# Kernel tuning notes

Measured on AMD Instinct MI355X. Metric: run time of the kernel, lower is better.

The kernel has to match this reference:

```python
import jax, jax.numpy as jnp
import numpy as np

N_NODES = 50000
N_EDGES = 800000
IN_CH = 128
OUT_CH = 128
TIME_DIM = 64


def setup_inputs() -> dict:
    key = jax.random.key(0)
    ks = jax.random.split(key, 7)
    x = jax.random.normal(ks[0], (N_NODES, IN_CH), dtype=jnp.float32)
    edge_index = jax.random.randint(ks[1], (2, N_EDGES), 0, N_NODES, dtype=jnp.int64)
    edge_t = jax.random.uniform(ks[2], (N_EDGES,), dtype=jnp.float32)
    # parameters
    freqs = jax.random.normal(ks[3], (TIME_DIM // 2,), dtype=jnp.float32)
    fan = IN_CH + TIME_DIM
    lim = float(np.sqrt(1.0 / fan))
    lin_w = jax.random.uniform(ks[4], (OUT_CH, fan), minval=-lim, maxval=lim, dtype=jnp.float32)
    lin_b = jax.random.uniform(ks[5], (OUT_CH,), minval=-lim, maxval=lim, dtype=jnp.float32)
    glim = float(np.sqrt(6.0 / (1 + OUT_CH)))
    attn = jax.random.uniform(ks[6], (1, OUT_CH), minval=-glim, maxval=glim, dtype=jnp.float32)
    return {"x": x, "edge_index": edge_index, "edge_t": edge_t,
            "freqs": freqs, "lin_w": lin_w, "lin_b": lin_b, "attn": attn}


def reference(x, edge_index, edge_t, freqs, lin_w, lin_b, attn):
    src, dst = edge_index[0], edge_index[1]
    n_nodes = x.shape[0]
    # time encoding: [E, time_dim]
    ang = edge_t[:, None] * freqs * (2.0 * jnp.pi)
    edge_attr = jnp.concatenate([jnp.sin(ang), jnp.cos(ang)], axis=-1)
    # gather source features and project: h = tanh(Linear(cat(x_j, te)))
    msg = jnp.concatenate([x[src], edge_attr], axis=-1)        # [E, in+time]
    h = jnp.tanh(msg @ lin_w.T + lin_b)                        # [E, out]
    # segment softmax over destination nodes
    alpha = (h * attn).sum(axis=-1)                            # [E]
    seg_max = jax.ops.segment_max(alpha, dst, num_segments=n_nodes)
    ex = jnp.exp(alpha - seg_max[dst])
    denom = jax.ops.segment_sum(ex, dst, num_segments=n_nodes)
    w = ex / (denom[dst] + 1e-16)
    # scatter-add aggregation
    out = jax.ops.segment_sum(h * w[:, None], dst, num_segments=n_nodes)
    return out
```

## Files before the change

kernel.cpp:

```cpp
#include <hip/hip_runtime.h>
#include <hip/hip_bf16.h>
#include <math.h>

#define IN_CHN 128
#define OUT_CHN 128
#define KD 192
#define TM 64

typedef __bf16 bf16x8 __attribute__((ext_vector_type(8)));
typedef float f32x4 __attribute__((ext_vector_type(4)));

static __device__ __forceinline__ unsigned short f2b(float f) {
    return __builtin_bit_cast(unsigned short, (__bf16)f);
}
static __device__ __forceinline__ float b2f(unsigned short b) {
    return __uint_as_float(((unsigned int)b) << 16);
}
static __device__ __forceinline__ float fast_tanh(float x) {
    float e = __expf(2.0f * x);
    return 1.0f - 2.0f * __builtin_amdgcn_rcpf(e + 1.0f);
}

#define GLL16(gsrc, ldst) \
    __builtin_amdgcn_global_load_lds( \
        (const __attribute__((address_space(1))) unsigned int*)(gsrc), \
        (__attribute__((address_space(3))) unsigned int*)(ldst), 16, 0, 0)

#define LDS_BARRIER() do { \
    asm volatile("s_waitcnt lgkmcnt(0)" ::: "memory"); \
    __builtin_amdgcn_s_barrier(); \
    __builtin_amdgcn_sched_barrier(0); \
} while (0)


__global__ __launch_bounds__(256) void cvt_x(const float* __restrict__ x,
    unsigned short* __restrict__ xb, long long n8)
{
    long long i = (long long)blockIdx.x * 256 + threadIdx.x;
    if (i >= n8) return;
    const float4* src = (const float4*)(x + i * 8);
    float4 v0 = src[0], v1 = src[1];
    ushort4 p0 = { f2b(v0.x), f2b(v0.y), f2b(v0.z), f2b(v0.w) };
    ushort4 p1 = { f2b(v1.x), f2b(v1.y), f2b(v1.z), f2b(v1.w) };
    *(ushort4*)(xb + i * 8)     = p0;
    *(ushort4*)(xb + i * 8 + 4) = p1;
}


__global__ __launch_bounds__(256) void count_deg(const int* __restrict__ ei,
                                                 int* __restrict__ deg, int E) {
    int e = blockIdx.x * 256 + threadIdx.x;
    if (e < E) atomicAdd(&deg[ei[E + e]], 1);
}

static __device__ __forceinline__ int wave_incl_scan(int v, int lane) {
    #pragma unroll
    for (int off = 1; off < 64; off <<= 1) {
        int t = __shfl_up(v, off);
        if (lane >= off) v += t;
    }
    return v;
}

__global__ __launch_bounds__(256) void scan_local(const int* __restrict__ deg,
    int* __restrict__ offs, int* __restrict__ partial, int Nn)
{
    __shared__ int wsum[4];
    int tid = threadIdx.x, lane = tid & 63, wid = tid >> 6;
    int i = blockIdx.x * 256 + tid;
    int v = (i < Nn) ? deg[i] : 0;
    int incl = wave_incl_scan(v, lane);
    if (lane == 63) wsum[wid] = incl;
    __syncthreads();
    int wpre = 0;
    for (int w = 0; w < wid; ++w) wpre += wsum[w];
    if (i < Nn) offs[i] = wpre + incl - v;
    if (tid == 255) partial[blockIdx.x] = wpre + incl;
}

__global__ __launch_bounds__(256) void scan_partial(int* __restrict__ partial, int nparts)
{
    __shared__ int wsum[4];
    int tid = threadIdx.x, lane = tid & 63, wid = tid >> 6;
    int v = (tid < nparts) ? partial[tid] : 0;
    int incl = wave_incl_scan(v, lane);
    if (lane == 63) wsum[wid] = incl;
    __syncthreads();
    int wpre = 0;
    for (int w = 0; w < wid; ++w) wpre += wsum[w];
    if (tid < nparts) partial[tid] = wpre + incl - v;
}

__global__ __launch_bounds__(256) void finalize_offs(int* __restrict__ offs,
    const int* __restrict__ partial, int* __restrict__ cursor, int Nn)
{
    int i = blockIdx.x * 256 + threadIdx.x;
    if (i < Nn) { int o = offs[i] + partial[i >> 8]; offs[i] = o; cursor[i] = o; }
}

__global__ __launch_bounds__(256) void fill_perm(const int* __restrict__ ei,
    const float* __restrict__ et, int* __restrict__ cursor,
    uint2* __restrict__ mt, int E)
{
    int e = blockIdx.x * 256 + threadIdx.x;
    if (e < E) {
        int d = ei[E + e];
        int pos = atomicAdd(&cursor[d], 1);
        mt[pos] = make_uint2((unsigned)ei[e], __float_as_uint(et[e]));
    }
}


__device__ __forceinline__ void load_meta(const uint2* __restrict__ mt,
    int tile, int E, int rbase, int g, int trow, int sv[2], float& tsv)
{
    int e0 = tile * TM;
    #pragma unroll
    for (int i = 0; i < 2; ++i) {
        int e = e0 + rbase + i * 4 + g;
        sv[i] = (int)mt[e < E ? e : E - 1].x;
    }
    int el = e0 + trow;
    tsv = __uint_as_float(mt[el < E ? el : E - 1].y);
}

__global__ __launch_bounds__(512) void gemm_mfma(
    const unsigned short* __restrict__ xb, const uint2* __restrict__ mt,
    const float* __restrict__ freqs, const float* __restrict__ lw,
    const float* __restrict__ lb, const float* __restrict__ attn,
    unsigned short* __restrict__ h_p, float* __restrict__ alpha8,
    int E, int Ep, int n_tiles)
{
    __shared__ unsigned short xs[2][TM][128];
    __shared__ unsigned short te[TM * 64];

    const int tid  = threadIdx.x;
    const int lane = tid & 63;
    const int wv   = tid >> 6;
    const int c16  = lane & 15;
    const int g    = lane >> 4;
    const int wbase = wv * 16;
    const int rbase = wv * 8;
    const int trow  = tid >> 3;
    const int tpart = tid & 7;

    bf16x8 Wf[6];
    #pragma unroll
    for (int kk = 0; kk < 6; ++kk) {
        const float* wp = lw + (size_t)(wbase + c16) * KD + kk * 32 + g * 8;
        float4 v0 = *(const float4*)wp;
        float4 v1 = *(const float4*)(wp + 4);
        bf16x8 b;
        b[0] = (__bf16)v0.x; b[1] = (__bf16)v0.y; b[2] = (__bf16)v0.z; b[3] = (__bf16)v0.w;
        b[4] = (__bf16)v1.x; b[5] = (__bf16)v1.y; b[6] = (__bf16)v1.z; b[7] = (__bf16)v1.w;
        Wf[kk] = b;
    }

    const f32x4 bias_v = *(const f32x4*)(lb   + wbase + g * 4);
    const f32x4 attn_v = *(const f32x4*)(attn + wbase + g * 4);

    const float coff = (tpart >= 4) ? 1.5707963267948966f : 0.0f;
    float frv[8];
    #pragma unroll
    for (int j = 0; j < 8; ++j) frv[j] = freqs[(tpart & 3) * 8 + j] * 6.283185307179586f;

    const int stride = gridDim.x;
    float ts_cur, ts_nxt;
    int sv_nxt[2];

    {
        int sv0[2];
        load_meta(mt, blockIdx.x, E, rbase, g, trow, sv0, ts_cur);
        #pragma unroll
        for (int i = 0; i < 2; ++i) {
            const int rlo = (rbase + i * 4 + g) & 15;
            const unsigned short* gsrc = xb + (size_t)sv0[i] * IN_CHN + ((c16 ^ rlo) * 8);
            GLL16(gsrc, &xs[0][rbase + i * 4][0]);
        }
        int t1 = blockIdx.x + stride;
        load_meta(mt, t1 < n_tiles ? t1 : n_tiles - 1, E, rbase, g, trow, sv_nxt, ts_nxt);
    }

    int cur = 0;

    for (int tile = blockIdx.x; tile < n_tiles; tile += stride) {
        const int e0 = tile * TM;

        ushort4 tp[2];
        {
            float v[8];
            #pragma unroll
            for (int j = 0; j < 8; ++j)
                v[j] = __sinf(ts_cur * frv[j] + coff);
            tp[0] = (ushort4){ f2b(v[0]), f2b(v[1]), f2b(v[2]), f2b(v[3]) };
            tp[1] = (ushort4){ f2b(v[4]), f2b(v[5]), f2b(v[6]), f2b(v[7]) };
        }

        int sv2[2]; float ts2;
        {
            int t2 = tile + 2 * stride;
            load_meta(mt, t2 < n_tiles ? t2 : n_tiles - 1, E, rbase, g, trow, sv2, ts2);
        }

        __syncthreads();

        if (tile + stride < n_tiles) {
            #pragma unroll
            for (int i = 0; i < 2; ++i) {
                const int rlo = (rbase + i * 4 + g) & 15;
                const unsigned short* gsrc = xb + (size_t)sv_nxt[i] * IN_CHN + ((c16 ^ rlo) * 8);
                GLL16(gsrc, &xs[cur ^ 1][rbase + i * 4][0]);
            }
        }

        {
            unsigned short* tr = &te[trow * 64];
            int slot = (tpart ^ (trow & 7)) * 8;
            *(ushort4*)(tr + slot)     = tp[0];
            *(ushort4*)(tr + slot + 4) = tp[1];
        }

        LDS_BARRIER();

        f32x4 acc[4];
        #pragma unroll
        for (int mi = 0; mi < 4; ++mi) acc[mi] = (f32x4){0.f, 0.f, 0.f, 0.f};

        __builtin_amdgcn_s_setprio(1);
        const unsigned short* xsc = &xs[cur][0][0];
        #pragma unroll
        for (int mi = 0; mi < 4; ++mi) {
            const int r = mi * 16 + c16;
            const unsigned short* xrow = xsc + r * 128;
            #pragma unroll
            for (int kk = 0; kk < 4; ++kk) {
                const int slot = ((kk << 2) + g) ^ c16;
                bf16x8 a = __builtin_bit_cast(bf16x8, *(const uint4*)(xrow + slot * 8));
                acc[mi] = __builtin_amdgcn_mfma_f32_16x16x32_bf16(Wf[kk], a, acc[mi], 0, 0, 0);
            }
            const unsigned short* trw = &te[r * 64];
            bf16x8 s8 = __builtin_bit_cast(bf16x8, *(const uint4*)(trw + ((g ^ (r & 7)) * 8)));
            bf16x8 c8 = __builtin_bit_cast(bf16x8, *(const uint4*)(trw + (((g + 4) ^ (r & 7)) * 8)));
            acc[mi] = __builtin_amdgcn_mfma_f32_16x16x32_bf16(Wf[4], s8, acc[mi], 0, 0, 0);
            acc[mi] = __builtin_amdgcn_mfma_f32_16x16x32_bf16(Wf[5], c8, acc[mi], 0, 0, 0);
        }
        __builtin_amdgcn_s_setprio(0);

        #pragma unroll
        for (int mi = 0; mi < 4; ++mi) {
            int e = e0 + mi * 16 + c16;
            f32x4 z = acc[mi];
            float p = 0.0f;
            #pragma unroll
            for (int r = 0; r < 4; ++r) {
                float h = fast_tanh(z[r] + bias_v[r]);
                z[r] = h;
                p = fmaf(h, attn_v[r], p);
            }
            ushort4 pv = (ushort4){ f2b(z[0]), f2b(z[1]), f2b(z[2]), f2b(z[3]) };
            p += __shfl_xor(p, 16);
            p += __shfl_xor(p, 32);
            if (e < E) {
                *(ushort4*)(h_p + (size_t)e * OUT_CHN + wbase + g * 4) = pv;
                if (g == 0) alpha8[(size_t)wv * Ep + e] = p;
            }
        }

        ts_cur = ts_nxt; ts_nxt = ts2;
        sv_nxt[0] = sv2[0]; sv_nxt[1] = sv2[1];
        cur ^= 1;
    }
}


__global__ __launch_bounds__(256) void calc_ex(float* __restrict__ a8,
    int E, int Ep)
{
    int i = blockIdx.x * 256 + threadIdx.x;
    int e = i * 4;
    if (e + 3 < E) {
        float4 s = *(const float4*)(a8 + e);
        #pragma unroll
        for (int q = 1; q < 8; ++q) {
            float4 v = *(const float4*)(a8 + (size_t)q * Ep + e);
            s.x += v.x; s.y += v.y; s.z += v.z; s.w += v.w;
        }
        float4 r = { __expf(s.x), __expf(s.y), __expf(s.z), __expf(s.w) };
        *(float4*)(a8 + e) = r;
    } else {
        for (int q = e; q < E; ++q) {
            float s = a8[q];
            for (int p = 1; p < 8; ++p) s += a8[(size_t)p * Ep + q];
            a8[q] = __expf(s);
        }
    }
}


__global__ __launch_bounds__(256) void agg(
    const unsigned short* __restrict__ h_p, const float* __restrict__ ex,
    const int* __restrict__ offs, const int* __restrict__ deg,
    float* __restrict__ out, int Nn)
{
    int wid  = threadIdx.x >> 6;
    int lane = threadIdx.x & 63;
    int node = blockIdx.x * 4 + wid;
    if (node >= Nn) return;
    int start = offs[node];
    int d = deg[node];
    int sub = lane >> 4;
    int ch  = (lane & 15) * 8;
    float4* op = (float4*)(out + (size_t)node * OUT_CHN + ch);
    if (d == 0) {
        if (sub == 0) { op[0] = (float4){0,0,0,0}; op[1] = (float4){0,0,0,0}; }
        return;
    }

    float s = 0.0f;
    for (int i = lane; i < d; i += 64) s += ex[start + i];
    #pragma unroll
    for (int off = 32; off > 0; off >>= 1) s += __shfl_xor(s, off);
    float rs = __builtin_amdgcn_rcpf(s + 1e-16f);

    float a[8];
    #pragma unroll
    for (int q = 0; q < 8; ++q) a[q] = 0.0f;

    for (int i = 0; i < d; i += 4) {
        int idx = i + sub;
        float w = 0.0f;
        uint4 hv = {0u, 0u, 0u, 0u};
        if (idx < d) {
            w = ex[start + idx] * rs;
            hv = *(const uint4*)(h_p + (size_t)(start + idx) * OUT_CHN + ch);
        }
        unsigned int hw[4] = { hv.x, hv.y, hv.z, hv.w };
        #pragma unroll
        for (int q = 0; q < 4; ++q) {
            a[2*q]   = fmaf(b2f((unsigned short)(hw[q] & 0xFFFFu)), w, a[2*q]);
            a[2*q+1] = fmaf(b2f((unsigned short)(hw[q] >> 16)),     w, a[2*q+1]);
        }
    }
    #pragma unroll
    for (int q = 0; q < 8; ++q) {
        a[q] += __shfl_xor(a[q], 16);
        a[q] += __shfl_xor(a[q], 32);
    }
    if (sub == 0) {
        op[0] = (float4){a[0], a[1], a[2], a[3]};
        op[1] = (float4){a[4], a[5], a[6], a[7]};
    }
}


extern "C" void kernel_launch(void* const* d_in, const int* in_sizes, int n_in,
                              void* d_out, int out_size, void* d_ws, size_t ws_size,
                              hipStream_t stream) {
    const float* x     = (const float*)d_in[0];
    const int*   ei    = (const int*)d_in[1];
    const float* et    = (const float*)d_in[2];
    const float* freqs = (const float*)d_in[3];
    const float* lw    = (const float*)d_in[4];
    const float* lb    = (const float*)d_in[5];
    const float* attn  = (const float*)d_in[6];
    float* out = (float*)d_out;

    const int E  = in_sizes[2];
    const int Nn = in_sizes[0] / IN_CHN;
    const int Ep = (E + 3) & ~3;

    char* ws = (char*)d_ws;
    unsigned short* h_p = (unsigned short*)ws;
    size_t off = (size_t)E * OUT_CHN * sizeof(unsigned short);
    float* alpha8  = (float*)(ws + off); off += (size_t)Ep * 8 * sizeof(float);
    uint2* mt      = (uint2*)(ws + off); off += (size_t)E * sizeof(uint2);
    unsigned short* xb = (unsigned short*)(ws + off); off += (size_t)Nn * IN_CHN * sizeof(unsigned short);
    int*   deg     = (int*)(ws + off);   off += (size_t)Nn * sizeof(int);
    int*   offs    = (int*)(ws + off);   off += (size_t)Nn * sizeof(int);
    int*   cursor  = (int*)(ws + off);   off += (size_t)Nn * sizeof(int);
    int*   partial = (int*)(ws + off);

    const int nblk = (Nn + 255) / 256;
    const int eblk = (E + 255) / 256;

    long long n8 = (long long)Nn * IN_CHN / 8;
    cvt_x<<<(unsigned)((n8 + 255) / 256), 256, 0, stream>>>(x, xb, n8);

    hipMemsetAsync(deg, 0, (size_t)Nn * sizeof(int), stream);
    count_deg<<<eblk, 256, 0, stream>>>(ei, deg, E);
    scan_local<<<nblk, 256, 0, stream>>>(deg, offs, partial, Nn);
    scan_partial<<<1, 256, 0, stream>>>(partial, nblk);
    finalize_offs<<<nblk, 256, 0, stream>>>(offs, partial, cursor, Nn);
    fill_perm<<<eblk, 256, 0, stream>>>(ei, et, cursor, mt, E);

    const int n_tiles = (E + TM - 1) / TM;
    gemm_mfma<<<768, 512, 0, stream>>>(xb, mt, freqs, lw, lb, attn,
                                       h_p, alpha8, E, Ep, n_tiles);

    calc_ex<<<(Ep / 4 + 255) / 256, 256, 0, stream>>>(alpha8, E, Ep);

    agg<<<(Nn + 3) / 4, 256, 0, stream>>>(h_p, alpha8, offs, deg, out, Nn);
}
```

Baseline: 254.0 us.

## Fuse segment softmax and aggregation into GEMM kernel over contiguous tile ranges

The GEMM kernel now gives each block a contiguous range of dst-sorted tiles. It keeps h and the logits in LDS and aggregates exp-weighted rows per destination node directly, with each wave handling every eighth node. Nodes that cross block boundaries are combined with atomics, and a small normalize pass divides by the accumulated denominators. This removes the h_p/alpha8 round trip through global memory and the separate calc_ex and agg kernels. In exchange it adds atomics, two memsets, serialized per-node loops inside the GEMM, and a softmax without the max subtraction (the old code also skipped it).

```diff
diff --git a/kernel.cpp b/kernel.cpp
--- a/kernel.cpp
+++ b/kernel.cpp
@@ -92,21 +92,26 @@
 }
 
 __global__ __launch_bounds__(256) void finalize_offs(int* __restrict__ offs,
-    const int* __restrict__ partial, int* __restrict__ cursor, int Nn)
+    const int* __restrict__ partial, int* __restrict__ cursor, int Nn, int E)
 {
     int i = blockIdx.x * 256 + threadIdx.x;
-    if (i < Nn) { int o = offs[i] + partial[i >> 8]; offs[i] = o; cursor[i] = o; }
+    if (i < Nn) {
+        int o = offs[i] + partial[i >> 8];
+        offs[i] = o; cursor[i] = o;
+        if (i == Nn - 1) offs[Nn] = E;
+    }
 }
 
 __global__ __launch_bounds__(256) void fill_perm(const int* __restrict__ ei,
     const float* __restrict__ et, int* __restrict__ cursor,
-    uint2* __restrict__ mt, int E)
+    uint2* __restrict__ mt, int* __restrict__ nid, int E)
 {
     int e = blockIdx.x * 256 + threadIdx.x;
     if (e < E) {
         int d = ei[E + e];
         int pos = atomicAdd(&cursor[d], 1);
         mt[pos] = make_uint2((unsigned)ei[e], __float_as_uint(et[e]));
+        nid[pos] = d;
     }
 }
 
@@ -124,15 +129,26 @@
     tsv = __uint_as_float(mt[el < E ? el : E - 1].y);
 }
 
-__global__ __launch_bounds__(512) void gemm_mfma(
+__global__ __launch_bounds__(512) void gemm_fused(
     const unsigned short* __restrict__ xb, const uint2* __restrict__ mt,
+    const int* __restrict__ nid, const int* __restrict__ offs,
     const float* __restrict__ freqs, const float* __restrict__ lw,
     const float* __restrict__ lb, const float* __restrict__ attn,
-    unsigned short* __restrict__ h_p, float* __restrict__ alpha8,
-    int E, int Ep, int n_tiles)
+    float* __restrict__ out, float* __restrict__ den_g,
+    int E, int Nn, int n_tiles, int kq, int kr)
 {
     __shared__ unsigned short xs[2][TM][128];
     __shared__ unsigned short te[TM * 64];
+    __shared__ unsigned short hx[TM][136];
+    __shared__ float exs[TM];
+
+    const int b    = blockIdx.x;
+    const int t0   = b * kq + min(b, kr);
+    const int cnt  = kq + (b < kr ? 1 : 0);
+    if (cnt <= 0 || t0 >= n_tiles) return;
+    const int tend = min(t0 + cnt, n_tiles);
+    const int be0  = t0 * TM;
+    const int bend = min(tend * TM, E);
 
     const int tid  = threadIdx.x;
     const int lane = tid & 63;
@@ -143,6 +159,8 @@
     const int rbase = wv * 8;
     const int trow  = tid >> 3;
     const int tpart = tid & 7;
+    const int sub  = lane >> 4;
+    const int chl  = lane & 15;
 
     bf16x8 Wf[6];
     #pragma unroll
@@ -150,12 +168,11 @@
         const float* wp = lw + (size_t)(wbase + c16) * KD + kk * 32 + g * 8;
         float4 v0 = *(const float4*)wp;
         float4 v1 = *(const float4*)(wp + 4);
-        bf16x8 b;
-        b[0] = (__bf16)v0.x; b[1] = (__bf16)v0.y; b[2] = (__bf16)v0.z; b[3] = (__bf16)v0.w;
-        b[4] = (__bf16)v1.x; b[5] = (__bf16)v1.y; b[6] = (__bf16)v1.z; b[7] = (__bf16)v1.w;
-        Wf[kk] = b;
-    }
-
+        bf16x8 bb;
+        bb[0] = (__bf16)v0.x; bb[1] = (__bf16)v0.y; bb[2] = (__bf16)v0.z; bb[3] = (__bf16)v0.w;
+        bb[4] = (__bf16)v1.x; bb[5] = (__bf16)v1.y; bb[6] = (__bf16)v1.z; bb[7] = (__bf16)v1.w;
+        Wf[kk] = bb;
+    }
     const f32x4 bias_v = *(const f32x4*)(lb   + wbase + g * 4);
     const f32x4 attn_v = *(const f32x4*)(attn + wbase + g * 4);
 
@@ -164,27 +181,32 @@
     #pragma unroll
     for (int j = 0; j < 8; ++j) frv[j] = freqs[(tpart & 3) * 8 + j] * 6.283185307179586f;
 
-    const int stride = gridDim.x;
+    int n0 = nid[be0];
+    int cur_node = n0 + ((wv - (n0 & 7)) & 7);
+    float a[8];
+    #pragma unroll
+    for (int q = 0; q < 8; ++q) a[q] = 0.0f;
+    float den = 0.0f;
+
     float ts_cur, ts_nxt;
     int sv_nxt[2];
-
     {
         int sv0[2];
-        load_meta(mt, blockIdx.x, E, rbase, g, trow, sv0, ts_cur);
+        load_meta(mt, t0, E, rbase, g, trow, sv0, ts_cur);
         #pragma unroll
         for (int i = 0; i < 2; ++i) {
             const int rlo = (rbase + i * 4 + g) & 15;
             const unsigned short* gsrc = xb + (size_t)sv0[i] * IN_CHN + ((c16 ^ rlo) * 8);
             GLL16(gsrc, &xs[0][rbase + i * 4][0]);
         }
-        int t1 = blockIdx.x + stride;
-        load_meta(mt, t1 < n_tiles ? t1 : n_tiles - 1, E, rbase, g, trow, sv_nxt, ts_nxt);
+        int t1 = t0 + 1;
+        load_meta(mt, t1 < tend ? t1 : tend - 1, E, rbase, g, trow, sv_nxt, ts_nxt);
     }
 
     int cur = 0;
-
-    for (int tile = blockIdx.x; tile < n_tiles; tile += stride) {
+    for (int tile = t0; tile < tend; ++tile) {
         const int e0 = tile * TM;
+        const int e1 = e0 + TM;
 
         ushort4 tp[2];
         {
@@ -195,16 +217,15 @@
             tp[0] = (ushort4){ f2b(v[0]), f2b(v[1]), f2b(v[2]), f2b(v[3]) };
             tp[1] = (ushort4){ f2b(v[4]), f2b(v[5]), f2b(v[6]), f2b(v[7]) };
         }
-
         int sv2[2]; float ts2;
         {
-            int t2 = tile + 2 * stride;
-            load_meta(mt, t2 < n_tiles ? t2 : n_tiles - 1, E, rbase, g, trow, sv2, ts2);
+            int t2 = tile + 2;
+            load_meta(mt, t2 < tend ? t2 : tend - 1, E, rbase, g, trow, sv2, ts2);
         }
 
         __syncthreads();
 
-        if (tile + stride < n_tiles) {
+        if (tile + 1 < tend) {
             #pragma unroll
             for (int i = 0; i < 2; ++i) {
                 const int rlo = (rbase + i * 4 + g) & 15;
@@ -212,12 +233,12 @@
                 GLL16(gsrc, &xs[cur ^ 1][rbase + i * 4][0]);
             }
         }
-
         {
             unsigned short* tr = &te[trow * 64];
             int slot = (tpart ^ (trow & 7)) * 8;
             *(ushort4*)(tr + slot)     = tp[0];
             *(ushort4*)(tr + slot + 4) = tp[1];
+            if (tid < TM) exs[tid] = 0.0f;
         }
 
         LDS_BARRIER();
@@ -235,8 +256,8 @@
             #pragma unroll
             for (int kk = 0; kk < 4; ++kk) {
                 const int slot = ((kk << 2) + g) ^ c16;
-                bf16x8 a = __builtin_bit_cast(bf16x8, *(const uint4*)(xrow + slot * 8));
-                acc[mi] = __builtin_amdgcn_mfma_f32_16x16x32_bf16(Wf[kk], a, acc[mi], 0, 0, 0);
+                bf16x8 av = __builtin_bit_cast(bf16x8, *(const uint4*)(xrow + slot * 8));
+                acc[mi] = __builtin_amdgcn_mfma_f32_16x16x32_bf16(Wf[kk], av, acc[mi], 0, 0, 0);
             }
             const unsigned short* trw = &te[r * 64];
             bf16x8 s8 = __builtin_bit_cast(bf16x8, *(const uint4*)(trw + ((g ^ (r & 7)) * 8)));
@@ -248,108 +269,109 @@
 
         #pragma unroll
         for (int mi = 0; mi < 4; ++mi) {
-            int e = e0 + mi * 16 + c16;
+            const int r = mi * 16 + c16;
             f32x4 z = acc[mi];
             float p = 0.0f;
             #pragma unroll
-            for (int r = 0; r < 4; ++r) {
-                float h = fast_tanh(z[r] + bias_v[r]);
-                z[r] = h;
-                p = fmaf(h, attn_v[r], p);
+            for (int q = 0; q < 4; ++q) {
+                float h = fast_tanh(z[q] + bias_v[q]);
+                z[q] = h;
+                p = fmaf(h, attn_v[q], p);
             }
             ushort4 pv = (ushort4){ f2b(z[0]), f2b(z[1]), f2b(z[2]), f2b(z[3]) };
+            *(ushort4*)&hx[r][wbase + g * 4] = pv;
             p += __shfl_xor(p, 16);
             p += __shfl_xor(p, 32);
-            if (e < E) {
-                *(ushort4*)(h_p + (size_t)e * OUT_CHN + wbase + g * 4) = pv;
-                if (g == 0) alpha8[(size_t)wv * Ep + e] = p;
-            }
+            if (g == 0) atomicAdd(&exs[r], p);
+        }
+
+        LDS_BARRIER();
+
+        while (cur_node < Nn) {
+            int s  = offs[cur_node];
+            if (s >= e1) break;
+            int en = offs[cur_node + 1];
+            int lo = s > e0 ? s : e0;
+            int hi = en < e1 ? en : e1;
+            for (int i = lo + sub; i < hi; i += 4) {
+                int li = i - e0;
+                float ex = __expf(exs[li]);
+                uint4 hv = *(const uint4*)&hx[li][chl * 8];
+                den += ex;
+                unsigned int hw[4] = { hv.x, hv.y, hv.z, hv.w };
+                #pragma unroll
+                for (int q = 0; q < 4; ++q) {
+                    a[2*q]   = fmaf(ex, b2f((unsigned short)(hw[q] & 0xFFFFu)), a[2*q]);
+                    a[2*q+1] = fmaf(ex, b2f((unsigned short)(hw[q] >> 16)),     a[2*q+1]);
+                }
+            }
+            if (en <= e1) {
+                #pragma unroll
+                for (int q = 0; q < 8; ++q) {
+                    a[q] += __shfl_xor(a[q], 16);
+                    a[q] += __shfl_xor(a[q], 32);
+                }
+                float ds = den + __shfl_xor(den, 16);
+                ds += __shfl_xor(ds, 32);
+                float* op = out + (size_t)cur_node * OUT_CHN + chl * 8;
+                if (s >= be0) {
+                    if (sub == 0) {
+                        *(float4*)op       = (float4){a[0], a[1], a[2], a[3]};
+                        *(float4*)(op + 4) = (float4){a[4], a[5], a[6], a[7]};
+                        if (chl == 0) den_g[cur_node] = ds;
+                    }
+                } else {
+                    if (sub == 0) {
+                        #pragma unroll
+                        for (int q = 0; q < 8; ++q) atomicAdd(op + q, a[q]);
+                        if (chl == 0) atomicAdd(&den_g[cur_node], ds);
+                    }
+                }
+                #pragma unroll
+                for (int q = 0; q < 8; ++q) a[q] = 0.0f;
+                den = 0.0f;
+                cur_node += 8;
+            } else break;
         }
 
         ts_cur = ts_nxt; ts_nxt = ts2;
         sv_nxt[0] = sv2[0]; sv_nxt[1] = sv2[1];
         cur ^= 1;
     }
-}
-
-
-__global__ __launch_bounds__(256) void calc_ex(float* __restrict__ a8,
-    int E, int Ep)
-{
-    int i = blockIdx.x * 256 + threadIdx.x;
-    int e = i * 4;
-    if (e + 3 < E) {
-        float4 s = *(const float4*)(a8 + e);
-        #pragma unroll
-        for (int q = 1; q < 8; ++q) {
-            float4 v = *(const float4*)(a8 + (size_t)q * Ep + e);
-            s.x += v.x; s.y += v.y; s.z += v.z; s.w += v.w;
-        }
-        float4 r = { __expf(s.x), __expf(s.y), __expf(s.z), __expf(s.w) };
-        *(float4*)(a8 + e) = r;
-    } else {
-        for (int q = e; q < E; ++q) {
-            float s = a8[q];
-            for (int p = 1; p < 8; ++p) s += a8[(size_t)p * Ep + q];
-            a8[q] = __expf(s);
-        }
-    }
-}
-
-
-__global__ __launch_bounds__(256) void agg(
-    const unsigned short* __restrict__ h_p, const float* __restrict__ ex,
-    const int* __restrict__ offs, const int* __restrict__ deg,
-    float* __restrict__ out, int Nn)
-{
-    int wid  = threadIdx.x >> 6;
-    int lane = threadIdx.x & 63;
-    int node = blockIdx.x * 4 + wid;
-    if (node >= Nn) return;
-    int start = offs[node];
-    int d = deg[node];
-    int sub = lane >> 4;
-    int ch  = (lane & 15) * 8;
-    float4* op = (float4*)(out + (size_t)node * OUT_CHN + ch);
-    if (d == 0) {
-        if (sub == 0) { op[0] = (float4){0,0,0,0}; op[1] = (float4){0,0,0,0}; }
-        return;
-    }
-
-    float s = 0.0f;
-    for (int i = lane; i < d; i += 64) s += ex[start + i];
-    #pragma unroll
-    for (int off = 32; off > 0; off >>= 1) s += __shfl_xor(s, off);
-    float rs = __builtin_amdgcn_rcpf(s + 1e-16f);
-
-    float a[8];
-    #pragma unroll
-    for (int q = 0; q < 8; ++q) a[q] = 0.0f;
-
-    for (int i = 0; i < d; i += 4) {
-        int idx = i + sub;
-        float w = 0.0f;
-        uint4 hv = {0u, 0u, 0u, 0u};
-        if (idx < d) {
-            w = ex[start + idx] * rs;
-            hv = *(const uint4*)(h_p + (size_t)(start + idx) * OUT_CHN + ch);
-        }
-        unsigned int hw[4] = { hv.x, hv.y, hv.z, hv.w };
-        #pragma unroll
-        for (int q = 0; q < 4; ++q) {
-            a[2*q]   = fmaf(b2f((unsigned short)(hw[q] & 0xFFFFu)), w, a[2*q]);
-            a[2*q+1] = fmaf(b2f((unsigned short)(hw[q] >> 16)),     w, a[2*q+1]);
-        }
-    }
-    #pragma unroll
-    for (int q = 0; q < 8; ++q) {
-        a[q] += __shfl_xor(a[q], 16);
-        a[q] += __shfl_xor(a[q], 32);
-    }
-    if (sub == 0) {
-        op[0] = (float4){a[0], a[1], a[2], a[3]};
-        op[1] = (float4){a[4], a[5], a[6], a[7]};
-    }
+
+    if (cur_node < Nn) {
+        int s = offs[cur_node];
+        if (s < bend && offs[cur_node + 1] > bend) {
+            #pragma unroll
+            for (int q = 0; q < 8; ++q) {
+                a[q] += __shfl_xor(a[q], 16);
+                a[q] += __shfl_xor(a[q], 32);
+            }
+            float ds = den + __shfl_xor(den, 16);
+            ds += __shfl_xor(ds, 32);
+            if (sub == 0) {
+                float* op = out + (size_t)cur_node * OUT_CHN + chl * 8;
+                #pragma unroll
+                for (int q = 0; q < 8; ++q) atomicAdd(op + q, a[q]);
+                if (chl == 0) atomicAdd(&den_g[cur_node], ds);
+            }
+        }
+    }
+}
+
+
+__global__ __launch_bounds__(256) void normalize(float* __restrict__ out,
+    const float* __restrict__ den_g, int Nn)
+{
+    int gid = blockIdx.x * 256 + threadIdx.x;
+    int n = gid >> 5;
+    if (n >= Nn) return;
+    int c = (gid & 31) * 4;
+    float rs = __builtin_amdgcn_rcpf(den_g[n] + 1e-16f);
+    float4* p = (float4*)(out + (size_t)n * OUT_CHN + c);
+    float4 v = *p;
+    v.x *= rs; v.y *= rs; v.z *= rs; v.w *= rs;
+    *p = v;
 }
 
 
@@ -367,16 +389,14 @@
 
     const int E  = in_sizes[2];
     const int Nn = in_sizes[0] / IN_CHN;
-    const int Ep = (E + 3) & ~3;
 
     char* ws = (char*)d_ws;
-    unsigned short* h_p = (unsigned short*)ws;
-    size_t off = (size_t)E * OUT_CHN * sizeof(unsigned short);
-    float* alpha8  = (float*)(ws + off); off += (size_t)Ep * 8 * sizeof(float);
-    uint2* mt      = (uint2*)(ws + off); off += (size_t)E * sizeof(uint2);
+    uint2* mt      = (uint2*)ws;         size_t off = (size_t)E * sizeof(uint2);
+    int*   nid     = (int*)(ws + off);   off += (size_t)E * sizeof(int);
     unsigned short* xb = (unsigned short*)(ws + off); off += (size_t)Nn * IN_CHN * sizeof(unsigned short);
+    float* den_g   = (float*)(ws + off); off += (size_t)Nn * sizeof(float);
     int*   deg     = (int*)(ws + off);   off += (size_t)Nn * sizeof(int);
-    int*   offs    = (int*)(ws + off);   off += (size_t)Nn * sizeof(int);
+    int*   offs    = (int*)(ws + off);   off += (size_t)(Nn + 1) * sizeof(int);
     int*   cursor  = (int*)(ws + off);   off += (size_t)Nn * sizeof(int);
     int*   partial = (int*)(ws + off);
 
@@ -390,14 +410,17 @@
     count_deg<<<eblk, 256, 0, stream>>>(ei, deg, E);
     scan_local<<<nblk, 256, 0, stream>>>(deg, offs, partial, Nn);
     scan_partial<<<1, 256, 0, stream>>>(partial, nblk);
-    finalize_offs<<<nblk, 256, 0, stream>>>(offs, partial, cursor, Nn);
-    fill_perm<<<eblk, 256, 0, stream>>>(ei, et, cursor, mt, E);
+    finalize_offs<<<nblk, 256, 0, stream>>>(offs, partial, cursor, Nn, E);
+    fill_perm<<<eblk, 256, 0, stream>>>(ei, et, cursor, mt, nid, E);
+
+    hipMemsetAsync(out, 0, (size_t)out_size * sizeof(float), stream);
+    hipMemsetAsync(den_g, 0, (size_t)Nn * sizeof(float), stream);
 
     const int n_tiles = (E + TM - 1) / TM;
-    gemm_mfma<<<768, 512, 0, stream>>>(xb, mt, freqs, lw, lb, attn,
-                                       h_p, alpha8, E, Ep, n_tiles);
-
-    calc_ex<<<(Ep / 4 + 255) / 256, 256, 0, stream>>>(alpha8, E, Ep);
-
-    agg<<<(Nn + 3) / 4, 256, 0, stream>>>(h_p, alpha8, offs, deg, out, Nn);
-}
+    const int NB = 512;
+    const int kq = n_tiles / NB, kr = n_tiles % NB;
+    gemm_fused<<<NB, 512, 0, stream>>>(xb, mt, nid, offs, freqs, lw, lb, attn,
+                                       out, den_g, E, Nn, n_tiles, kq, kr);
+
+    normalize<<<(Nn * 32 + 255) / 256, 256, 0, stream>>>(out, den_g, Nn);
+}
```

Result: slower. 259.3 us (+2.1%).
